# Performance work log

Hardware: AMD Instinct MI355X
Metric: run time of the kernel (lower is better)

The kernel has to match this reference:

```python
import jax, jax.numpy as jnp
import numpy as np


def setup_inputs() -> dict:
    key = jax.random.key(0)
    ks = jax.random.split(key, 6)
    B, N, D, A = 4, 512, 768, 128
    matrix = jax.random.normal(ks[0], (B, N, D), dtype=jnp.float32)
    mask = jax.random.randint(ks[1], (B, N, N, 1), 0, 2, dtype=jnp.int32)
    W1_w = jax.random.normal(ks[2], (D, A), dtype=jnp.float32) * (1.0 / np.sqrt(D))
    W1_b = jnp.zeros((A,), dtype=jnp.float32)
    W2_w = jax.random.normal(ks[3], (D, A), dtype=jnp.float32) * (1.0 / np.sqrt(D))
    W2_b = jnp.zeros((A,), dtype=jnp.float32)
    v_w = jax.random.normal(ks[4], (A, 1), dtype=jnp.float32) * (1.0 / np.sqrt(A))
    return {"matrix": matrix, "mask": mask, "W1_w": W1_w, "W1_b": W1_b,
            "W2_w": W2_w, "W2_b": W2_b, "v_w": v_w}


def reference(matrix, mask, W1_w, W1_b, W2_w, W2_b, v_w):
    # matrix: [B,N,D]; mask: [B,N,N,1]
    w1 = matrix @ W1_w + W1_b                     # [B,N,A] (query-side proj)
    w2 = matrix @ W2_w + W2_b                     # [B,N,A] (key-side proj)
    # pairwise additive scores: v . tanh(w1_i + w2_j) -> [B,N,N]
    pair = jnp.tanh(w1[:, :, None, :] + w2[:, None, :, :])  # [B,N,N,A]
    scores = jnp.einsum('bija,ao->bij', pair, v_w)           # [B,N,N]
    boolean_mask = mask[..., 0].astype(bool)                  # [B,N,N]
    neg = jnp.finfo(scores.dtype).min
    masked = jnp.where(boolean_mask, scores, neg)
    attn = jax.nn.softmax(masked, axis=-1)
    attn = jnp.where(jnp.isnan(attn), jnp.zeros((), attn.dtype), attn)
    return attn @ matrix                          # [B,N,D]
```

## Files before the change

### kernel.cpp

```cpp
#include <hip/hip_runtime.h>

#define B_ 4
#define N_ 512
#define D_ 768
#define A_ 128

typedef short bf16x8 __attribute__((ext_vector_type(8)));
typedef ushort u16x8 __attribute__((ext_vector_type(8)));
typedef float f32x4 __attribute__((ext_vector_type(4)));

__device__ __forceinline__ ushort f2h(float x) {
  uint u = __builtin_bit_cast(uint, x);
  return (ushort)((u + 0x7fffu + ((u >> 16) & 1u)) >> 16);
}
__device__ __forceinline__ float h2f(ushort h) {
  uint u = ((uint)h) << 16;
  return __builtin_bit_cast(float, u);
}
__device__ __forceinline__ bf16x8 ld8(const ushort* p) {
  return *(const bf16x8*)p;
}
#define MFMA(a, b, c) __builtin_amdgcn_mfma_f32_16x16x32_bf16(a, b, c, 0, 0, 0)

__global__ __launch_bounds__(256) void k0_prep(
    const float* __restrict__ M, const float* __restrict__ W1,
    const float* __restrict__ W2, const float* __restrict__ vw,
    ushort* __restrict__ Mr_h, ushort* __restrict__ Mr_l,
    ushort* __restrict__ Mt_h, ushort* __restrict__ Mt_l,
    ushort* __restrict__ Wt_h, ushort* __restrict__ Wt_l,
    float* __restrict__ uvec) {
  __shared__ ushort lds_h[64][40];
  __shared__ ushort lds_l[64][40];
  const int t = threadIdx.x;
  const int bid = blockIdx.x;
  if (bid < 768) {
    const int dq = bid % 12;
    const int rest = bid / 12;
    const int d0 = dq * 64;
    const int n0 = (rest & 15) * 32;
    const int b = rest >> 4;
    const int n = t >> 3;
    const int dg = (t & 7) * 8;
    const size_t roff = ((size_t)(b * N_ + n0 + n)) * D_ + d0 + dg;
    const float4 v0 = *(const float4*)(M + roff);
    const float4 v1 = *(const float4*)(M + roff + 4);
    const float x[8] = {v0.x, v0.y, v0.z, v0.w, v1.x, v1.y, v1.z, v1.w};
    u16x8 vh, vl;
#pragma unroll
    for (int e = 0; e < 8; ++e) {
      ushort h = f2h(x[e]);
      ushort l = f2h(x[e] - h2f(h));
      vh[e] = h;
      vl[e] = l;
      lds_h[dg + e][n] = h;
      lds_l[dg + e][n] = l;
    }
    *(u16x8*)(Mr_h + roff) = vh;
    *(u16x8*)(Mr_l + roff) = vl;
    __syncthreads();
    const int dd = t >> 2;
    const int ng = (t & 3) * 8;
    const size_t toff = ((size_t)b * D_ + d0 + dd) * N_ + n0 + ng;
    *(u16x8*)(Mt_h + toff) = *(const u16x8*)(&lds_h[dd][ng]);
    *(u16x8*)(Mt_l + toff) = *(const u16x8*)(&lds_l[dd][ng]);
  } else {
    const int c = t;
    const int k0 = (bid - 768) * 8;
    const float* __restrict__ Wp = (c < A_) ? W1 : W2;
    const int cc = c & (A_ - 1);
    u16x8 vh, vl;
#pragma unroll
    for (int e = 0; e < 8; ++e) {
      float x = Wp[(size_t)(k0 + e) * A_ + cc];
      ushort h = f2h(x);
      vh[e] = h;
      vl[e] = f2h(x - h2f(h));
    }
    *(u16x8*)(Wt_h + (size_t)c * D_ + k0) = vh;
    *(u16x8*)(Wt_l + (size_t)c * D_ + k0) = vl;
    if (bid == 768 && c < A_) uvec[c] = -2.f * vw[c];
  }
}

__global__ __launch_bounds__(256) void k1_mfma(
    const ushort* __restrict__ Mr_h, const ushort* __restrict__ Mr_l,
    const ushort* __restrict__ Wt_h, const ushort* __restrict__ Wt_l,
    const float* __restrict__ b1, const float* __restrict__ b2,
    float* __restrict__ w1e, float* __restrict__ w2e) {
  __shared__ float l_red[4][32][33];
  const int t = threadIdx.x;
  const int l = t & 63;
  const int w = t >> 6;
  const int r = l & 15, g = l >> 4;
  const int row0 = blockIdx.x * 32;
  const int cb = blockIdx.y * 32;
  const int kbase = w * 192;
  const size_t oA = (size_t)(row0 + r) * D_ + kbase + g * 8;
  const size_t oA2 = oA + (size_t)16 * D_;
  const size_t oB = (size_t)(cb + r) * D_ + kbase + g * 8;
  const size_t oB2 = oB + (size_t)16 * D_;
  f32x4 acc[2][2] = {};
  bf16x8 A[2][4], Bv[2][4];
#define K1LOAD(s, k0)                                                        \
  A[s][0] = ld8(Mr_h + oA + (k0));  A[s][1] = ld8(Mr_h + oA2 + (k0));        \
  A[s][2] = ld8(Mr_l + oA + (k0));  A[s][3] = ld8(Mr_l + oA2 + (k0));        \
  Bv[s][0] = ld8(Wt_h + oB + (k0)); Bv[s][1] = ld8(Wt_h + oB2 + (k0));       \
  Bv[s][2] = ld8(Wt_l + oB + (k0)); Bv[s][3] = ld8(Wt_l + oB2 + (k0));
#define K1MM(s)                                                              \
  acc[0][0] = MFMA(A[s][0], Bv[s][0], acc[0][0]);                            \
  acc[0][0] = MFMA(A[s][0], Bv[s][2], acc[0][0]);                            \
  acc[0][0] = MFMA(A[s][2], Bv[s][0], acc[0][0]);                            \
  acc[0][1] = MFMA(A[s][0], Bv[s][1], acc[0][1]);                            \
  acc[0][1] = MFMA(A[s][0], Bv[s][3], acc[0][1]);                            \
  acc[0][1] = MFMA(A[s][2], Bv[s][1], acc[0][1]);                            \
  acc[1][0] = MFMA(A[s][1], Bv[s][0], acc[1][0]);                            \
  acc[1][0] = MFMA(A[s][1], Bv[s][2], acc[1][0]);                            \
  acc[1][0] = MFMA(A[s][3], Bv[s][0], acc[1][0]);                            \
  acc[1][1] = MFMA(A[s][1], Bv[s][1], acc[1][1]);                            \
  acc[1][1] = MFMA(A[s][1], Bv[s][3], acc[1][1]);                            \
  acc[1][1] = MFMA(A[s][3], Bv[s][1], acc[1][1]);
  K1LOAD(0, 0)
#pragma unroll
  for (int kt = 0; kt < 6; ++kt) {
    if (kt & 1) {
      if (kt < 5) { K1LOAD(0, (kt + 1) * 32) }
      K1MM(1)
    } else {
      if (kt < 5) { K1LOAD(1, (kt + 1) * 32) }
      K1MM(0)
    }
  }
#undef K1LOAD
#undef K1MM
#pragma unroll
  for (int fi = 0; fi < 2; ++fi)
#pragma unroll
    for (int fj = 0; fj < 2; ++fj)
#pragma unroll
      for (int rr = 0; rr < 4; ++rr)
        l_red[w][fi * 16 + g * 4 + rr][fj * 16 + r] = acc[fi][fj][rr];
  __syncthreads();

  const float SC = 2.8853900817779268f;
  const int b = row0 >> 9;
  const int n0 = row0 & (N_ - 1);
  if (cb < A_) {
#pragma unroll
    for (int k = 0; k < 4; ++k) {
      const int row = (t >> 5) + k * 8;
      const int col = t & 31;
      float v = l_red[0][row][col] + l_red[1][row][col] +
                l_red[2][row][col] + l_red[3][row][col];
      v = (v + b1[cb + col]) * SC;
      w1e[(size_t)(row0 + row) * A_ + cb + col] = __builtin_amdgcn_exp2f(v);
    }
  } else {
#pragma unroll
    for (int k = 0; k < 4; ++k) {
      const int row = t & 31;
      const int col = (t >> 5) + k * 8;
      float v = l_red[0][row][col] + l_red[1][row][col] +
                l_red[2][row][col] + l_red[3][row][col];
      v = (v + b2[cb - A_ + col]) * SC;
      w2e[(size_t)(b * A_ + cb - A_ + col) * N_ + n0 + row] =
          __builtin_amdgcn_exp2f(v);
    }
  }
}

__global__ __launch_bounds__(512) void k2_scores(
    const float* __restrict__ w1e, const float* __restrict__ w2e,
    const float* __restrict__ uvec, const int* __restrict__ mask,
    const float* __restrict__ vw, ushort* __restrict__ ah,
    ushort* __restrict__ al) {
  __shared__ float l_w2[2][16][N_];
  const int t = threadIdx.x;
  const int lane = t & 63;
  const int w = t >> 6;
  const int i0 = blockIdx.x * 8;
  const int b = i0 >> 9;
  const int i = i0 + w;
  const float* __restrict__ w1row = w1e + (size_t)i * A_;

  float vs = vw[lane] + vw[64 + lane];
#pragma unroll
  for (int off = 32; off; off >>= 1) vs += __shfl_xor(vs, off);

  const float* __restrict__ w2src = w2e + (size_t)b * A_ * N_;
  float4 st[4];

#define STAGE_LOAD(cc)                                                      \
  {                                                                         \
    const float* __restrict__ src = w2src + (size_t)(cc) * 16 * N_;         \
    _Pragma("unroll") for (int k = 0; k < 4; ++k) {                         \
      const int f = t + k * 512;                                            \
      st[k] = *(const float4*)(src + (size_t)(f >> 7) * N_ + (f & 127) * 4);\
    }                                                                       \
  }
#define STAGE_WRITE(bf)                                                     \
  {                                                                         \
    _Pragma("unroll") for (int k = 0; k < 4; ++k) {                         \
      const int f = t + k * 512;                                            \
      *(float4*)(&l_w2[bf][f >> 7][(f & 127) * 4]) = st[k];                 \
    }                                                                       \
  }

  STAGE_LOAD(0)
  STAGE_WRITE(0)
  __syncthreads();

  float s[8] = {};
#pragma unroll 1
  for (int cc = 0; cc < 8; ++cc) {
    if (cc + 1 < 8) STAGE_LOAD(cc + 1)
    const float(*wb)[N_] = l_w2[cc & 1];
#pragma unroll 1
    for (int aa = 0; aa < 4; ++aa) {
      const float4 wa = *(const float4*)(w1row + cc * 16 + aa * 4);
      const float4 uu = *(const float4*)(uvec + cc * 16 + aa * 4);
#pragma unroll
      for (int jt = 0; jt < 8; ++jt) {
        const int jj = jt * 64 + lane;
        const float x0 = wb[aa * 4 + 0][jj];
        const float x1 = wb[aa * 4 + 1][jj];
        const float x2 = wb[aa * 4 + 2][jj];
        const float x3 = wb[aa * 4 + 3][jj];
        float acc = s[jt];
        acc = fmaf(uu.x, __builtin_amdgcn_rcpf(fmaf(wa.x, x0, 1.f)), acc);
        acc = fmaf(uu.y, __builtin_amdgcn_rcpf(fmaf(wa.y, x1, 1.f)), acc);
        acc = fmaf(uu.z, __builtin_amdgcn_rcpf(fmaf(wa.z, x2, 1.f)), acc);
        acc = fmaf(uu.w, __builtin_amdgcn_rcpf(fmaf(wa.w, x3, 1.f)), acc);
        s[jt] = acc;
      }
    }
    if (cc + 1 < 8) { STAGE_WRITE((cc + 1) & 1) }
    __syncthreads();
  }
#undef STAGE_LOAD
#undef STAGE_WRITE

  const float NEG = -3.402823466e38f;
#pragma unroll
  for (int jt = 0; jt < 8; ++jt) {
    const int mk = mask[(size_t)i * N_ + jt * 64 + lane];
    s[jt] = mk ? (vs + s[jt]) : NEG;
  }

  float rmax = s[0];
#pragma unroll
  for (int jt = 1; jt < 8; ++jt) rmax = fmaxf(rmax, s[jt]);
#pragma unroll
  for (int off = 32; off; off >>= 1) rmax = fmaxf(rmax, __shfl_xor(rmax, off));
  const float L2E = 1.4426950408889634f;
  float psum = 0.f;
#pragma unroll
  for (int jt = 0; jt < 8; ++jt) {
    s[jt] = __builtin_amdgcn_exp2f((s[jt] - rmax) * L2E);
    psum += s[jt];
  }
#pragma unroll
  for (int off = 32; off; off >>= 1) psum += __shfl_xor(psum, off);
  const float inv = __builtin_amdgcn_rcpf(psum);
#pragma unroll
  for (int jt = 0; jt < 8; ++jt) {
    const float pv = s[jt] * inv;
    const ushort hh = f2h(pv);
    ah[(size_t)i * N_ + jt * 64 + lane] = hh;
    al[(size_t)i * N_ + jt * 64 + lane] = f2h(pv - h2f(hh));
  }
}

__global__ __launch_bounds__(256) void k3_mfma(
    const ushort* __restrict__ ah, const ushort* __restrict__ al,
    const ushort* __restrict__ Mt_h, const ushort* __restrict__ Mt_l,
    float* __restrict__ out) {
  __shared__ float l_red[4][64][33];
  const int t = threadIdx.x;
  const int l = t & 63;
  const int w = t >> 6;
  const int r = l & 15, g = l >> 4;
  const int row0 = blockIdx.x * 64;
  const int d0 = blockIdx.y * 32;
  const int b = row0 >> 9;
  const int jbase = w * 128;
  const ushort* __restrict__ Bh = Mt_h + (size_t)b * D_ * N_;
  const ushort* __restrict__ Bl = Mt_l + (size_t)b * D_ * N_;
  size_t oA[4];
#pragma unroll
  for (int fi = 0; fi < 4; ++fi)
    oA[fi] = (size_t)(row0 + fi * 16 + r) * N_ + jbase + g * 8;
  const size_t oB = (size_t)(d0 + r) * N_ + jbase + g * 8;
  const size_t oB2 = oB + (size_t)16 * N_;
  f32x4 acc[4][2] = {};
  bf16x8 A[2][8], Bv[2][4];
#define K3LOAD(s, j0)                                                        \
  A[s][0] = ld8(ah + oA[0] + (j0)); A[s][1] = ld8(ah + oA[1] + (j0));        \
  A[s][2] = ld8(ah + oA[2] + (j0)); A[s][3] = ld8(ah + oA[3] + (j0));        \
  A[s][4] = ld8(al + oA[0] + (j0)); A[s][5] = ld8(al + oA[1] + (j0));        \
  A[s][6] = ld8(al + oA[2] + (j0)); A[s][7] = ld8(al + oA[3] + (j0));        \
  Bv[s][0] = ld8(Bh + oB + (j0));   Bv[s][1] = ld8(Bh + oB2 + (j0));         \
  Bv[s][2] = ld8(Bl + oB + (j0));   Bv[s][3] = ld8(Bl + oB2 + (j0));
#define K3MM(s)                                                              \
  _Pragma("unroll") for (int fi = 0; fi < 4; ++fi)                           \
  _Pragma("unroll") for (int fd = 0; fd < 2; ++fd) {                         \
    acc[fi][fd] = MFMA(A[s][fi], Bv[s][fd], acc[fi][fd]);                    \
    acc[fi][fd] = MFMA(A[s][fi], Bv[s][fd + 2], acc[fi][fd]);                \
    acc[fi][fd] = MFMA(A[s][fi + 4], Bv[s][fd], acc[fi][fd]);                \
  }
  K3LOAD(0, 0)
#pragma unroll
  for (int kt = 0; kt < 4; ++kt) {
    if (kt & 1) {
      if (kt < 3) { K3LOAD(0, (kt + 1) * 32) }
      K3MM(1)
    } else {
      if (kt < 3) { K3LOAD(1, (kt + 1) * 32) }
      K3MM(0)
    }
  }
#undef K3LOAD
#undef K3MM
#pragma unroll
  for (int fi = 0; fi < 4; ++fi)
#pragma unroll
    for (int fd = 0; fd < 2; ++fd)
#pragma unroll
      for (int rr = 0; rr < 4; ++rr)
        l_red[w][fi * 16 + g * 4 + rr][fd * 16 + r] = acc[fi][fd][rr];
  __syncthreads();
#pragma unroll
  for (int k = 0; k < 8; ++k) {
    const int row = (t >> 5) + k * 8;
    const int col = t & 31;
    const float v = l_red[0][row][col] + l_red[1][row][col] +
                    l_red[2][row][col] + l_red[3][row][col];
    out[(size_t)(row0 + row) * D_ + d0 + col] = v;
  }
}

extern "C" void kernel_launch(void* const* d_in, const int* in_sizes, int n_in,
                              void* d_out, int out_size, void* d_ws,
                              size_t ws_size, hipStream_t stream) {
  const float* M = (const float*)d_in[0];
  const int* mask = (const int*)d_in[1];
  const float* W1 = (const float*)d_in[2];
  const float* b1 = (const float*)d_in[3];
  const float* W2 = (const float*)d_in[4];
  const float* b2 = (const float*)d_in[5];
  const float* vw = (const float*)d_in[6];
  float* out = (float*)d_out;

  float* w1e = (float*)d_ws;
  float* w2e = w1e + 2048 * A_;
  ushort* ah = (ushort*)(w2e + 4 * A_ * N_);
  ushort* al = ah + 2048 * N_;
  ushort* Mr_h = al + 2048 * N_;
  ushort* Mr_l = Mr_h + 2048 * D_;
  ushort* Mt_h = Mr_l + 2048 * D_;
  ushort* Mt_l = Mt_h + 2048 * D_;
  ushort* Wt_h = Mt_l + 2048 * D_;
  ushort* Wt_l = Wt_h + 256 * D_;
  float* uvec = (float*)(Wt_l + 256 * D_);

  k0_prep<<<864, 256, 0, stream>>>(M, W1, W2, vw, Mr_h, Mr_l, Mt_h, Mt_l,
                                   Wt_h, Wt_l, uvec);
  k1_mfma<<<dim3(2048 / 32, 8), 256, 0, stream>>>(Mr_h, Mr_l, Wt_h, Wt_l,
                                                  b1, b2, w1e, w2e);
  k2_scores<<<(B_ * N_) / 8, 512, 0, stream>>>(w1e, w2e, uvec, mask, vw,
                                               ah, al);
  k3_mfma<<<dim3(2048 / 64, D_ / 32), 256, 0, stream>>>(ah, al, Mt_h, Mt_l,
                                                        out);
}
```

Measured before the change: 80.04 us.

## Split each score row across two waves with vectorized LDS loads and LDS softmax reduction

```diff
diff --git a/kernel.cpp b/kernel.cpp
--- a/kernel.cpp
+++ b/kernel.cpp
@@ -7,6 +7,7 @@
 
 typedef short bf16x8 __attribute__((ext_vector_type(8)));
 typedef ushort u16x8 __attribute__((ext_vector_type(8)));
+typedef ushort u16x4 __attribute__((ext_vector_type(4)));
 typedef float f32x4 __attribute__((ext_vector_type(4)));
 
 __device__ __forceinline__ ushort f2h(float x) {
@@ -168,39 +169,44 @@
   }
 }
 
-__global__ __launch_bounds__(512) void k2_scores(
+__global__ __launch_bounds__(1024) void k2_scores(
     const float* __restrict__ w1e, const float* __restrict__ w2e,
     const float* __restrict__ uvec, const int* __restrict__ mask,
     const float* __restrict__ vw, ushort* __restrict__ ah,
     ushort* __restrict__ al) {
   __shared__ float l_w2[2][16][N_];
+  __shared__ float l_red[8][2];
+  __shared__ float l_sum[8][2];
   const int t = threadIdx.x;
   const int lane = t & 63;
   const int w = t >> 6;
+  const int r = w >> 1;
+  const int h = w & 1;
   const int i0 = blockIdx.x * 8;
   const int b = i0 >> 9;
-  const int i = i0 + w;
-  const float* __restrict__ w1row = w1e + (size_t)i * A_;
+  const int i = i0 + r;
+  const int iu = __builtin_amdgcn_readfirstlane(i);
+  const float* __restrict__ w1row = w1e + (size_t)iu * A_;
 
   float vs = vw[lane] + vw[64 + lane];
 #pragma unroll
   for (int off = 32; off; off >>= 1) vs += __shfl_xor(vs, off);
 
   const float* __restrict__ w2src = w2e + (size_t)b * A_ * N_;
-  float4 st[4];
+  float4 st[2];
 
 #define STAGE_LOAD(cc)                                                      \
   {                                                                         \
     const float* __restrict__ src = w2src + (size_t)(cc) * 16 * N_;         \
-    _Pragma("unroll") for (int k = 0; k < 4; ++k) {                         \
-      const int f = t + k * 512;                                            \
+    _Pragma("unroll") for (int k = 0; k < 2; ++k) {                         \
+      const int f = t + k * 1024;                                           \
       st[k] = *(const float4*)(src + (size_t)(f >> 7) * N_ + (f & 127) * 4);\
     }                                                                       \
   }
 #define STAGE_WRITE(bf)                                                     \
   {                                                                         \
-    _Pragma("unroll") for (int k = 0; k < 4; ++k) {                         \
-      const int f = t + k * 512;                                            \
+    _Pragma("unroll") for (int k = 0; k < 2; ++k) {                         \
+      const int f = t + k * 1024;                                           \
       *(float4*)(&l_w2[bf][f >> 7][(f & 127) * 4]) = st[k];                 \
     }                                                                       \
   }
@@ -209,7 +215,8 @@
   STAGE_WRITE(0)
   __syncthreads();
 
-  float s[8] = {};
+  const int jb = h * 256 + lane * 4;
+  float4 s = {0.f, 0.f, 0.f, 0.f};
 #pragma unroll 1
   for (int cc = 0; cc < 8; ++cc) {
     if (cc + 1 < 8) STAGE_LOAD(cc + 1)
@@ -218,19 +225,17 @@
     for (int aa = 0; aa < 4; ++aa) {
       const float4 wa = *(const float4*)(w1row + cc * 16 + aa * 4);
       const float4 uu = *(const float4*)(uvec + cc * 16 + aa * 4);
-#pragma unroll
-      for (int jt = 0; jt < 8; ++jt) {
-        const int jj = jt * 64 + lane;
-        const float x0 = wb[aa * 4 + 0][jj];
-        const float x1 = wb[aa * 4 + 1][jj];
-        const float x2 = wb[aa * 4 + 2][jj];
-        const float x3 = wb[aa * 4 + 3][jj];
-        float acc = s[jt];
-        acc = fmaf(uu.x, __builtin_amdgcn_rcpf(fmaf(wa.x, x0, 1.f)), acc);
-        acc = fmaf(uu.y, __builtin_amdgcn_rcpf(fmaf(wa.y, x1, 1.f)), acc);
-        acc = fmaf(uu.z, __builtin_amdgcn_rcpf(fmaf(wa.z, x2, 1.f)), acc);
-        acc = fmaf(uu.w, __builtin_amdgcn_rcpf(fmaf(wa.w, x3, 1.f)), acc);
-        s[jt] = acc;
+      const float wa_[4] = {wa.x, wa.y, wa.z, wa.w};
+      const float uu_[4] = {uu.x, uu.y, uu.z, uu.w};
+#pragma unroll
+      for (int e = 0; e < 4; ++e) {
+        const float wx = wa_[e];
+        const float ux = uu_[e];
+        const float4 x = *(const float4*)(&wb[aa * 4 + e][jb]);
+        s.x = fmaf(ux, __builtin_amdgcn_rcpf(fmaf(wx, x.x, 1.f)), s.x);
+        s.y = fmaf(ux, __builtin_amdgcn_rcpf(fmaf(wx, x.y, 1.f)), s.y);
+        s.z = fmaf(ux, __builtin_amdgcn_rcpf(fmaf(wx, x.z, 1.f)), s.z);
+        s.w = fmaf(ux, __builtin_amdgcn_rcpf(fmaf(wx, x.w, 1.f)), s.w);
       }
     }
     if (cc + 1 < 8) { STAGE_WRITE((cc + 1) & 1) }
@@ -240,34 +245,41 @@
 #undef STAGE_WRITE
 
   const float NEG = -3.402823466e38f;
-#pragma unroll
-  for (int jt = 0; jt < 8; ++jt) {
-    const int mk = mask[(size_t)i * N_ + jt * 64 + lane];
-    s[jt] = mk ? (vs + s[jt]) : NEG;
-  }
-
-  float rmax = s[0];
-#pragma unroll
-  for (int jt = 1; jt < 8; ++jt) rmax = fmaxf(rmax, s[jt]);
+  const int4 mk = *(const int4*)(mask + (size_t)i * N_ + jb);
+  s.x = mk.x ? (vs + s.x) : NEG;
+  s.y = mk.y ? (vs + s.y) : NEG;
+  s.z = mk.z ? (vs + s.z) : NEG;
+  s.w = mk.w ? (vs + s.w) : NEG;
+
+  float rmax = fmaxf(fmaxf(s.x, s.y), fmaxf(s.z, s.w));
 #pragma unroll
   for (int off = 32; off; off >>= 1) rmax = fmaxf(rmax, __shfl_xor(rmax, off));
+  if (lane == 0) l_red[r][h] = rmax;
+  __syncthreads();
+  rmax = fmaxf(l_red[r][0], l_red[r][1]);
+
   const float L2E = 1.4426950408889634f;
-  float psum = 0.f;
-#pragma unroll
-  for (int jt = 0; jt < 8; ++jt) {
-    s[jt] = __builtin_amdgcn_exp2f((s[jt] - rmax) * L2E);
-    psum += s[jt];
-  }
+  s.x = __builtin_amdgcn_exp2f((s.x - rmax) * L2E);
+  s.y = __builtin_amdgcn_exp2f((s.y - rmax) * L2E);
+  s.z = __builtin_amdgcn_exp2f((s.z - rmax) * L2E);
+  s.w = __builtin_amdgcn_exp2f((s.w - rmax) * L2E);
+  float psum = (s.x + s.y) + (s.z + s.w);
 #pragma unroll
   for (int off = 32; off; off >>= 1) psum += __shfl_xor(psum, off);
-  const float inv = __builtin_amdgcn_rcpf(psum);
-#pragma unroll
-  for (int jt = 0; jt < 8; ++jt) {
-    const float pv = s[jt] * inv;
-    const ushort hh = f2h(pv);
-    ah[(size_t)i * N_ + jt * 64 + lane] = hh;
-    al[(size_t)i * N_ + jt * 64 + lane] = f2h(pv - h2f(hh));
-  }
+  if (lane == 0) l_sum[r][h] = psum;
+  __syncthreads();
+  const float inv = __builtin_amdgcn_rcpf(l_sum[r][0] + l_sum[r][1]);
+
+  const float p[4] = {s.x * inv, s.y * inv, s.z * inv, s.w * inv};
+  u16x4 vh, vl;
+#pragma unroll
+  for (int e = 0; e < 4; ++e) {
+    const ushort hh = f2h(p[e]);
+    vh[e] = hh;
+    vl[e] = f2h(p[e] - h2f(hh));
+  }
+  *(u16x4*)(ah + (size_t)i * N_ + jb) = vh;
+  *(u16x4*)(al + (size_t)i * N_ + jb) = vl;
 }
 
 __global__ __launch_bounds__(256) void k3_mfma(
@@ -366,8 +378,8 @@
                                    Wt_h, Wt_l, uvec);
   k1_mfma<<<dim3(2048 / 32, 8), 256, 0, stream>>>(Mr_h, Mr_l, Wt_h, Wt_l,
                                                   b1, b2, w1e, w2e);
-  k2_scores<<<(B_ * N_) / 8, 512, 0, stream>>>(w1e, w2e, uvec, mask, vw,
-                                               ah, al);
+  k2_scores<<<(B_ * N_) / 8, 1024, 0, stream>>>(w1e, w2e, uvec, mask, vw,
+                                                ah, al);
   k3_mfma<<<dim3(2048 / 64, D_ / 32), 256, 0, stream>>>(ah, al, Mt_h, Mt_l,
                                                         out);
 }
```

Result: faster. 69.95 us (-12.6%).
